# Kernel optimization log

Measured on AMD Instinct MI355X. Metric: run time of the kernel, lower is better.

The kernel has to match this reference:

```python
import jax, jax.numpy as jnp
import numpy as np
from jax import lax

IOU_THRESHOLD = 0.2  # hardcoded in TinyModel.forward
N = 8192


def setup_inputs() -> dict:
    key = jax.random.key(0)
    k1, k2, k3 = jax.random.split(key, 3)
    # Build valid boxes: top-left corner in [0, 1000), size in [1, 51)
    xy = jax.random.uniform(k1, (N, 2), dtype=jnp.float32) * 1000.0
    wh = jax.random.uniform(k2, (N, 2), dtype=jnp.float32) * 50.0 + 1.0
    rois = jnp.concatenate([xy, xy + wh], axis=-1)  # [N,4] = (x1,y1,x2,y2)
    scores = jax.random.uniform(k3, (N,), dtype=jnp.float32)
    return {"rois": rois, "scores": scores}


def _pairwise_iou(boxes):
    # boxes: [N,4]; returns [N,N] IoU (torchvision convention, no +1)
    x1, y1, x2, y2 = boxes[:, 0], boxes[:, 1], boxes[:, 2], boxes[:, 3]
    area = (x2 - x1) * (y2 - y1)                       # [N]
    ix1 = jnp.maximum(x1[:, None], x1[None, :])
    iy1 = jnp.maximum(y1[:, None], y1[None, :])
    ix2 = jnp.minimum(x2[:, None], x2[None, :])
    iy2 = jnp.minimum(y2[:, None], y2[None, :])
    iw = jnp.clip(ix2 - ix1, 0.0)
    ih = jnp.clip(iy2 - iy1, 0.0)
    inter = iw * ih                                    # [N,N]
    union = area[:, None] + area[None, :] - inter
    return inter / jnp.maximum(union, 1e-9)


def _nms_keep_mask(rois, scores, thr):
    n = rois.shape[0]
    order = jnp.argsort(-scores)                       # descending by score
    boxes = rois[order]                                # [N,4] sorted
    over = _pairwise_iou(boxes) > thr                  # [N,N] bool
    idx = jnp.arange(n)
    # box i may only suppress lower-scored boxes j > i (strict upper triangle)
    over = over & (idx[None, :] > idx[:, None])

    def body(i, keep):
        row = over[i] & keep[i]                        # suppress only if i survives
        return keep & ~row

    keep_sorted = lax.fori_loop(0, n, body, jnp.ones((n,), dtype=bool))
    # scatter back to original box ordering
    keep = jnp.zeros((n,), dtype=bool).at[order].set(keep_sorted)
    return keep


def reference(rois, scores):
    # NMS returns a data-dependent set of kept indices in torch; for fixed
    # shapes we return the scores with suppressed boxes zeroed (original order).
    keep = _nms_keep_mask(rois, scores, IOU_THRESHOLD)  # [N] bool
    return jnp.where(keep, scores, 0.0)
```

## Files before the change

kernel.cpp:

```cpp
#include <hip/hip_runtime.h>

#define N 8192
#define CAP 64
#define THR 0.2f

__global__ __launch_bounds__(256) void rank_kernel(const float* __restrict__ scores,
                                                   unsigned* __restrict__ rank) {
    __shared__ float s[1024];
    const int jbase = blockIdx.y * 1024;
    for (int t = threadIdx.x; t < 1024; t += 256) s[t] = scores[jbase + t];
    __syncthreads();
    const int i = blockIdx.x * 256 + threadIdx.x;
    const float si = scores[i];
    unsigned c = 0;
    #pragma unroll 8
    for (int jj = 0; jj < 1024; ++jj) {
        float sj = s[jj];
        int j = jbase + jj;
        c += (sj > si) || (sj == si && j < i);
    }
    atomicAdd(&rank[i], c);
}

__global__ __launch_bounds__(256) void scatter_kernel(const float* __restrict__ rois,
                                                      const unsigned* __restrict__ rank,
                                                      unsigned* __restrict__ order,
                                                      float4* __restrict__ sboxes) {
    const int i = blockIdx.x * 256 + threadIdx.x;
    const unsigned r = rank[i];
    order[r] = (unsigned)i;
    sboxes[r] = ((const float4*)rois)[i];
}

__device__ __forceinline__ bool iou_over(const float4 A, const float4 B) {
    float areaA = __fmul_rn(__fsub_rn(A.z, A.x), __fsub_rn(A.w, A.y));
    float areaB = __fmul_rn(__fsub_rn(B.z, B.x), __fsub_rn(B.w, B.y));
    float ix1 = fmaxf(A.x, B.x);
    float iy1 = fmaxf(A.y, B.y);
    float ix2 = fminf(A.z, B.z);
    float iy2 = fminf(A.w, B.w);
    float iw = fmaxf(__fsub_rn(ix2, ix1), 0.0f);
    float ih = fmaxf(__fsub_rn(iy2, iy1), 0.0f);
    float inter = __fmul_rn(iw, ih);
    float uni = __fsub_rn(__fadd_rn(areaA, areaB), inter);
    float iou = __fdiv_rn(inter, fmaxf(uni, 1e-9f));
    return iou > THR;
}

__global__ __launch_bounds__(256) void edge_kernel(const float4* __restrict__ sboxes,
                                                   unsigned long long* __restrict__ premask,
                                                   unsigned* __restrict__ cnt,
                                                   unsigned short* __restrict__ edgesTS,
                                                   unsigned short* __restrict__ edgesOvf) {
    const int k = blockIdx.x;
    int ti = (int)((257.0f - sqrtf(66049.0f - 8.0f * (float)k)) * 0.5f);
    if (ti > 127) ti = 127;
    if (ti < 0) ti = 0;
    while (ti < 127 && (128 * (ti + 1) - ((ti + 1) * ti) / 2) <= k) ++ti;
    while (ti > 0 && (128 * ti - (ti * (ti - 1)) / 2) > k) --ti;
    const int tj = ti + (k - (128 * ti - (ti * (ti - 1)) / 2));

    __shared__ float4 rb[64], cb[64];
    const int t = threadIdx.x;
    if (t < 64) rb[t] = sboxes[ti * 64 + t];
    else if (t < 128) cb[t - 64] = sboxes[tj * 64 + (t - 64)];
    __syncthreads();
    #pragma unroll
    for (int kk = 0; kk < 16; ++kk) {
        int p = kk * 256 + t;
        int r = p >> 6, c = p & 63;
        int is = ti * 64 + r, js = tj * 64 + c;
        if (js <= is) continue;
        if (iou_over(rb[r], cb[c])) {
            if (ti == tj) {
                atomicOr(&premask[js], 1ull << r);
            } else {
                unsigned pos = atomicAdd(&cnt[is], 1u);
                if (pos < 8) {
                    edgesTS[(((is >> 6) * 2 + (pos >> 2)) * 64 + (is & 63)) * 4 + (pos & 3)] =
                        (unsigned short)js;
                } else if (pos < CAP) {
                    edgesOvf[(size_t)is * 56 + (pos - 8)] = (unsigned short)js;
                }
            }
        }
    }
}


#define PF(B, CH) do { \
    int ch_ = (CH); \
    if (ch_ < 128) { \
        int pb_ = ch_ * 64 + lane; \
        pm##B = premask[pb_]; \
        n##B  = cnt[pb_]; \
        ea##B = edgesT[(ch_ * 2 + 0) * 64 + lane]; \
        eb##B = edgesT[(ch_ * 2 + 1) * 64 + lane]; \
    } \
} while (0)

#define APPLY(i, W, SH) { \
    unsigned d_ = (unsigned)((W) >> (SH)) & 0xFFFFu; \
    bool v_ = (i) < nn_; \
    unsigned a_ = v_ ? (d_ >> 5) : (unsigned)lane; \
    unsigned m_ = v_ ? ~(1u << (d_ & 31)) : ~0u; \
    atomicAnd(&alive[a_], m_); }

#define STEP(B, C) do { \
    const unsigned av_ = (alive[(C) * 2 + (lane >> 5)] >> (lane & 31)) & 1u; \
    unsigned long long anz = __ballot(pm##B != 0ull); \
    unsigned long long kept = __ballot(av_ != 0u); \
    if (anz != 0ull) { \
        bool mydec = !av_ || (pm##B == 0ull); \
        unsigned long long decided = __ballot(mydec); \
        kept = __ballot(av_ && (pm##B == 0ull)); \
        while (decided != ~0ull) { \
            bool ready = !mydec && ((pm##B & ~decided) == 0ull); \
            bool k_ = ready && ((pm##B & kept) == 0ull); \
            kept |= __ballot(k_); \
            decided |= __ballot(ready); \
            mydec = mydec || ready; \
        } \
    } \
    if (lane == 0) keptw[(C)] = kept; \
    const unsigned kb_ = (unsigned)(kept >> lane) & 1u; \
    unsigned nn_ = kb_ ? (n##B > 8u ? 8u : n##B) : 0u; \
    APPLY(0u, ea##B, 0)  APPLY(1u, ea##B, 16) APPLY(2u, ea##B, 32) APPLY(3u, ea##B, 48) \
    APPLY(4u, eb##B, 0)  APPLY(5u, eb##B, 16) APPLY(6u, eb##B, 32) APPLY(7u, eb##B, 48) \
    if (__any(kb_ && n##B > 8u)) { \
        unsigned nf_ = kb_ ? (n##B > CAP ? (unsigned)CAP : n##B) : 0u; \
        for (unsigned e_ = 8; e_ < nf_; ++e_) { \
            unsigned d_ = edgesOvf[(size_t)((C) * 64 + lane) * 56 + (e_ - 8)]; \
            atomicAnd(&alive[d_ >> 5], ~(1u << (d_ & 31))); \
        } \
    } \
    PF(B, (C) + 8); \
    asm volatile("s_waitcnt lgkmcnt(0)" ::: "memory"); \
} while (0)

__global__ __launch_bounds__(64) void resolve_kernel(const unsigned long long* __restrict__ premask,
                                                     const unsigned* __restrict__ cnt,
                                                     const unsigned long long* __restrict__ edgesT,
                                                     const unsigned short* __restrict__ edgesOvf,
                                                     unsigned long long* __restrict__ keptw) {
    __shared__ unsigned alive[256];
    const int lane = threadIdx.x;
    #pragma unroll
    for (int w = 0; w < 4; ++w) alive[w * 64 + lane] = 0xFFFFFFFFu;
    asm volatile("s_waitcnt lgkmcnt(0)" ::: "memory");

    unsigned long long pm0, pm1, pm2, pm3, pm4, pm5, pm6, pm7;
    unsigned n0, n1, n2, n3, n4, n5, n6, n7;
    unsigned long long ea0, ea1, ea2, ea3, ea4, ea5, ea6, ea7;
    unsigned long long eb0, eb1, eb2, eb3, eb4, eb5, eb6, eb7;

    PF(0, 0); PF(1, 1); PF(2, 2); PF(3, 3);
    PF(4, 4); PF(5, 5); PF(6, 6); PF(7, 7);

    for (int cc = 0; cc < 128; cc += 8) {
        STEP(0, cc + 0); STEP(1, cc + 1); STEP(2, cc + 2); STEP(3, cc + 3);
        STEP(4, cc + 4); STEP(5, cc + 5); STEP(6, cc + 6); STEP(7, cc + 7);
    }
}

__global__ __launch_bounds__(256) void out_kernel(const float* __restrict__ scores,
                                                  const unsigned* __restrict__ order,
                                                  const unsigned long long* __restrict__ keptw,
                                                  float* __restrict__ out) {
    const int s = blockIdx.x * 256 + threadIdx.x;
    const unsigned orig = order[s];
    const unsigned keep = (unsigned)((keptw[s >> 6] >> (s & 63)) & 1ull);
    out[orig] = keep ? scores[orig] : 0.0f;
}

extern "C" void kernel_launch(void* const* d_in, const int* in_sizes, int n_in,
                              void* d_out, int out_size, void* d_ws, size_t ws_size,
                              hipStream_t stream) {
    const float* rois   = (const float*)d_in[0];
    const float* scores = (const float*)d_in[1];
    float* out = (float*)d_out;

    char* ws = (char*)d_ws;
    unsigned*            rank     = (unsigned*)(ws);
    unsigned*            cnt      = (unsigned*)(ws + 32768);
    unsigned long long*  premask  = (unsigned long long*)(ws + 65536);
    unsigned*            order    = (unsigned*)(ws + 131072);
    float4*              sboxes   = (float4*)(ws + 163840);
    unsigned long long*  keptw    = (unsigned long long*)(ws + 294912);
    unsigned long long*  edgesT   = (unsigned long long*)(ws + 295936);
    unsigned short*      edgesOvf = (unsigned short*)(ws + 427008);

    hipMemsetAsync(ws, 0, 131072, stream);

    rank_kernel<<<dim3(32, 8), 256, 0, stream>>>(scores, rank);
    scatter_kernel<<<32, 256, 0, stream>>>(rois, rank, order, sboxes);
    edge_kernel<<<8256, 256, 0, stream>>>(sboxes, premask, cnt,
                                          (unsigned short*)edgesT, edgesOvf);
    resolve_kernel<<<1, 64, 0, stream>>>(premask, cnt, edgesT, edgesOvf, keptw);
    out_kernel<<<32, 256, 0, stream>>>(scores, order, keptw, out);
}
```

Baseline: 132.8 us.

## Fuse NMS pipeline into one persistent kernel with grid-wide barriers

Replaces the memset plus five separate launches (rank, scatter, edge, resolve, output) with a single persistent kernel of 512 blocks. Stages are separated by atomic-counter grid barriers, and workspace zeroing moves into the kernel. The rank and scatter steps are merged, and the final output write is folded into the single-wave resolve stage using a kept-mask held in shared memory. The aim is to remove launch and inter-kernel gaps. The cost is spin-waiting barriers, which assume all 512 blocks are co-resident. The output scatter is also now done by one wavefront instead of 32 blocks.

```diff
diff --git a/kernel.cpp b/kernel.cpp
--- a/kernel.cpp
+++ b/kernel.cpp
@@ -1,36 +1,10 @@
 #include <hip/hip_runtime.h>
 
 #define N 8192
+#define NBLK 512
 #define CAP 64
 #define THR 0.2f
 
-__global__ __launch_bounds__(256) void rank_kernel(const float* __restrict__ scores,
-                                                   unsigned* __restrict__ rank) {
-    __shared__ float s[1024];
-    const int jbase = blockIdx.y * 1024;
-    for (int t = threadIdx.x; t < 1024; t += 256) s[t] = scores[jbase + t];
-    __syncthreads();
-    const int i = blockIdx.x * 256 + threadIdx.x;
-    const float si = scores[i];
-    unsigned c = 0;
-    #pragma unroll 8
-    for (int jj = 0; jj < 1024; ++jj) {
-        float sj = s[jj];
-        int j = jbase + jj;
-        c += (sj > si) || (sj == si && j < i);
-    }
-    atomicAdd(&rank[i], c);
-}
-
-__global__ __launch_bounds__(256) void scatter_kernel(const float* __restrict__ rois,
-                                                      const unsigned* __restrict__ rank,
-                                                      unsigned* __restrict__ order,
-                                                      float4* __restrict__ sboxes) {
-    const int i = blockIdx.x * 256 + threadIdx.x;
-    const unsigned r = rank[i];
-    order[r] = (unsigned)i;
-    sboxes[r] = ((const float4*)rois)[i];
-}
 
 __device__ __forceinline__ bool iou_over(const float4 A, const float4 B) {
     float areaA = __fmul_rn(__fsub_rn(A.z, A.x), __fsub_rn(A.w, A.y));
@@ -47,52 +21,26 @@
     return iou > THR;
 }
 
-__global__ __launch_bounds__(256) void edge_kernel(const float4* __restrict__ sboxes,
-                                                   unsigned long long* __restrict__ premask,
-                                                   unsigned* __restrict__ cnt,
-                                                   unsigned short* __restrict__ edgesTS,
-                                                   unsigned short* __restrict__ edgesOvf) {
-    const int k = blockIdx.x;
-    int ti = (int)((257.0f - sqrtf(66049.0f - 8.0f * (float)k)) * 0.5f);
-    if (ti > 127) ti = 127;
-    if (ti < 0) ti = 0;
-    while (ti < 127 && (128 * (ti + 1) - ((ti + 1) * ti) / 2) <= k) ++ti;
-    while (ti > 0 && (128 * ti - (ti * (ti - 1)) / 2) > k) --ti;
-    const int tj = ti + (k - (128 * ti - (ti * (ti - 1)) / 2));
-
-    __shared__ float4 rb[64], cb[64];
-    const int t = threadIdx.x;
-    if (t < 64) rb[t] = sboxes[ti * 64 + t];
-    else if (t < 128) cb[t - 64] = sboxes[tj * 64 + (t - 64)];
+__device__ __forceinline__ void bar_arrive(unsigned* bar) {
+    __threadfence();
     __syncthreads();
-    #pragma unroll
-    for (int kk = 0; kk < 16; ++kk) {
-        int p = kk * 256 + t;
-        int r = p >> 6, c = p & 63;
-        int is = ti * 64 + r, js = tj * 64 + c;
-        if (js <= is) continue;
-        if (iou_over(rb[r], cb[c])) {
-            if (ti == tj) {
-                atomicOr(&premask[js], 1ull << r);
-            } else {
-                unsigned pos = atomicAdd(&cnt[is], 1u);
-                if (pos < 8) {
-                    edgesTS[(((is >> 6) * 2 + (pos >> 2)) * 64 + (is & 63)) * 4 + (pos & 3)] =
-                        (unsigned short)js;
-                } else if (pos < CAP) {
-                    edgesOvf[(size_t)is * 56 + (pos - 8)] = (unsigned short)js;
-                }
-            }
-        }
-    }
-}
-
+    if (threadIdx.x == 0)
+        __hip_atomic_fetch_add(bar, 1u, __ATOMIC_RELEASE, __HIP_MEMORY_SCOPE_AGENT);
+}
+__device__ __forceinline__ void bar_wait(unsigned* bar, unsigned target) {
+    if (threadIdx.x == 0) {
+        while (__hip_atomic_load(bar, __ATOMIC_ACQUIRE, __HIP_MEMORY_SCOPE_AGENT) < target)
+            __builtin_amdgcn_s_sleep(8);
+    }
+    __syncthreads();
+    (void)__hip_atomic_load(bar, __ATOMIC_ACQUIRE, __HIP_MEMORY_SCOPE_AGENT);
+}
 
 #define PF(B, CH) do { \
     int ch_ = (CH); \
     if (ch_ < 128) { \
         int pb_ = ch_ * 64 + lane; \
-        pm##B = premask[pb_]; \
+        pm##B = prem[pb_]; \
         n##B  = cnt[pb_]; \
         ea##B = edgesT[(ch_ * 2 + 0) * 64 + lane]; \
         eb##B = edgesT[(ch_ * 2 + 1) * 64 + lane]; \
@@ -122,7 +70,7 @@
             mydec = mydec || ready; \
         } \
     } \
-    if (lane == 0) keptw[(C)] = kept; \
+    if (lane == 0) keptL[(C)] = kept; \
     const unsigned kb_ = (unsigned)(kept >> lane) & 1u; \
     unsigned nn_ = kb_ ? (n##B > 8u ? 8u : n##B) : 0u; \
     APPLY(0u, ea##B, 0)  APPLY(1u, ea##B, 16) APPLY(2u, ea##B, 32) APPLY(3u, ea##B, 48) \
@@ -138,13 +86,110 @@
     asm volatile("s_waitcnt lgkmcnt(0)" ::: "memory"); \
 } while (0)
 
-__global__ __launch_bounds__(64) void resolve_kernel(const unsigned long long* __restrict__ premask,
-                                                     const unsigned* __restrict__ cnt,
-                                                     const unsigned long long* __restrict__ edgesT,
-                                                     const unsigned short* __restrict__ edgesOvf,
-                                                     unsigned long long* __restrict__ keptw) {
+__global__ __launch_bounds__(256, 2)
+void mega_kernel(const float* __restrict__ rois,
+                 const float* __restrict__ scores,
+                 float* __restrict__ out,
+                 unsigned* bar,
+                 unsigned* cnt,
+                 unsigned long long* prem,
+                 unsigned* order,
+                 float4* sboxes,
+                 unsigned long long* edgesT,
+                 unsigned short* edgesOvf) {
+    __shared__ float sc[1024];
+    __shared__ unsigned part[256];
+    __shared__ float4 rb[64], cb[64];
     __shared__ unsigned alive[256];
-    const int lane = threadIdx.x;
+    __shared__ unsigned long long keptL[128];
+
+    const int t = threadIdx.x;
+    const int b = blockIdx.x;
+    const int gtid = b * 256 + t;
+
+    {
+        unsigned* z = cnt;
+        if (gtid < 8192) z[gtid] = 0u;
+        unsigned* pz = (unsigned*)prem;
+        if (gtid < 16384) pz[gtid] = 0u;
+    }
+
+    {
+        const int ib  = b * 16;
+        const int il  = t >> 4;
+        const int i   = ib + il;
+        const int sub = t & 15;
+        const float si = scores[i];
+        unsigned c = 0;
+        for (int tile = 0; tile < 8; ++tile) {
+            ((float4*)sc)[t] = ((const float4*)scores)[tile * 256 + t];
+            __syncthreads();
+            const int j0 = sub * 64;
+            #pragma unroll 16
+            for (int q = 0; q < 64; ++q) {
+                int jj = j0 + q;
+                float sj = sc[jj];
+                int j = tile * 1024 + jj;
+                c += (sj > si) || (sj == si && j < i);
+            }
+            __syncthreads();
+        }
+        part[t] = c;
+        __syncthreads();
+        if (t < 16) {
+            const int i2 = ib + t;
+            unsigned r = 0;
+            #pragma unroll
+            for (int q = 0; q < 16; ++q) r += part[t * 16 + q];
+            order[r] = (unsigned)i2;
+            sboxes[r] = ((const float4*)rois)[i2];
+        }
+    }
+
+    bar_arrive(bar);
+    bar_wait(bar, NBLK);
+
+    unsigned short* edgesTS = (unsigned short*)edgesT;
+    for (int p = b; p < 8256; p += NBLK) {
+        int ti = (int)((257.0f - sqrtf(66049.0f - 8.0f * (float)p)) * 0.5f);
+        if (ti > 127) ti = 127;
+        if (ti < 0) ti = 0;
+        while (ti < 127 && (128 * (ti + 1) - ((ti + 1) * ti) / 2) <= p) ++ti;
+        while (ti > 0 && (128 * ti - (ti * (ti - 1)) / 2) > p) --ti;
+        const int tj = ti + (p - (128 * ti - (ti * (ti - 1)) / 2));
+
+        if (t < 64) rb[t] = sboxes[ti * 64 + t];
+        else if (t < 128) cb[t - 64] = sboxes[tj * 64 + (t - 64)];
+        __syncthreads();
+        #pragma unroll
+        for (int kk = 0; kk < 16; ++kk) {
+            int pp = kk * 256 + t;
+            int r = pp >> 6, c = pp & 63;
+            int is = ti * 64 + r, js = tj * 64 + c;
+            if (js <= is) continue;
+            if (iou_over(rb[r], cb[c])) {
+                if (ti == tj) {
+                    atomicOr(&prem[js], 1ull << r);
+                } else {
+                    unsigned pos = atomicAdd(&cnt[is], 1u);
+                    if (pos < 8) {
+                        edgesTS[(((is >> 6) * 2 + (pos >> 2)) * 64 + (is & 63)) * 4 + (pos & 3)] =
+                            (unsigned short)js;
+                    } else if (pos < CAP) {
+                        edgesOvf[(size_t)is * 56 + (pos - 8)] = (unsigned short)js;
+                    }
+                }
+            }
+        }
+        __syncthreads();
+    }
+
+    bar_arrive(bar);
+    if (b != 0) return;
+    bar_wait(bar, 2 * NBLK);
+    if (t >= 64) return;
+
+    const int lane = t;
     #pragma unroll
     for (int w = 0; w < 4; ++w) alive[w * 64 + lane] = 0xFFFFFFFFu;
     asm volatile("s_waitcnt lgkmcnt(0)" ::: "memory");
@@ -161,16 +206,15 @@
         STEP(0, cc + 0); STEP(1, cc + 1); STEP(2, cc + 2); STEP(3, cc + 3);
         STEP(4, cc + 4); STEP(5, cc + 5); STEP(6, cc + 6); STEP(7, cc + 7);
     }
-}
-
-__global__ __launch_bounds__(256) void out_kernel(const float* __restrict__ scores,
-                                                  const unsigned* __restrict__ order,
-                                                  const unsigned long long* __restrict__ keptw,
-                                                  float* __restrict__ out) {
-    const int s = blockIdx.x * 256 + threadIdx.x;
-    const unsigned orig = order[s];
-    const unsigned keep = (unsigned)((keptw[s >> 6] >> (s & 63)) & 1ull);
-    out[orig] = keep ? scores[orig] : 0.0f;
+
+    #pragma unroll 8
+    for (int q = 0; q < 128; ++q) {
+        int s = q * 64 + lane;
+        unsigned long long kw = keptL[q];
+        unsigned orig = order[s];
+        float v = ((kw >> lane) & 1ull) ? scores[orig] : 0.0f;
+        out[orig] = v;
+    }
 }
 
 extern "C" void kernel_launch(void* const* d_in, const int* in_sizes, int n_in,
@@ -181,21 +225,16 @@
     float* out = (float*)d_out;
 
     char* ws = (char*)d_ws;
-    unsigned*            rank     = (unsigned*)(ws);
-    unsigned*            cnt      = (unsigned*)(ws + 32768);
-    unsigned long long*  premask  = (unsigned long long*)(ws + 65536);
-    unsigned*            order    = (unsigned*)(ws + 131072);
-    float4*              sboxes   = (float4*)(ws + 163840);
-    unsigned long long*  keptw    = (unsigned long long*)(ws + 294912);
-    unsigned long long*  edgesT   = (unsigned long long*)(ws + 295936);
-    unsigned short*      edgesOvf = (unsigned short*)(ws + 427008);
-
-    hipMemsetAsync(ws, 0, 131072, stream);
-
-    rank_kernel<<<dim3(32, 8), 256, 0, stream>>>(scores, rank);
-    scatter_kernel<<<32, 256, 0, stream>>>(rois, rank, order, sboxes);
-    edge_kernel<<<8256, 256, 0, stream>>>(sboxes, premask, cnt,
-                                          (unsigned short*)edgesT, edgesOvf);
-    resolve_kernel<<<1, 64, 0, stream>>>(premask, cnt, edgesT, edgesOvf, keptw);
-    out_kernel<<<32, 256, 0, stream>>>(scores, order, keptw, out);
-}
+    unsigned*            bar      = (unsigned*)(ws);
+    unsigned*            cnt      = (unsigned*)(ws + 256);
+    unsigned long long*  prem     = (unsigned long long*)(ws + 33024);
+    unsigned*            order    = (unsigned*)(ws + 98560);
+    float4*              sboxes   = (float4*)(ws + 131328);
+    unsigned long long*  edgesT   = (unsigned long long*)(ws + 262400);
+    unsigned short*      edgesOvf = (unsigned short*)(ws + 393472);
+
+    hipMemsetAsync(ws, 0, 256, stream);
+
+    mega_kernel<<<NBLK, 256, 0, stream>>>(rois, scores, out, bar, cnt, prem,
+                                          order, sboxes, edgesT, edgesOvf);
+}
```

Result: slower. 312.3 us (+135.2%).

## Resolve 256-box groups via in-register bitmask chains and fuse output scatter

Applied to the files above, without the earlier changes.

Edges between boxes in the same 256-box group now go to a 4-word per-box bitmask instead of the sparse edge lists. The single-wave resolver can then handle four 64-box chunks per step, chaining kept masks with ballots rather than doing atomic alive-bit updates through LDS. It also removes one launch by folding the output kernel into the resolver. The costs are a larger memset, more work inside the serial single-wave kernel for the output pass, and higher register pressure.

```diff
diff --git a/kernel.cpp b/kernel.cpp
--- a/kernel.cpp
+++ b/kernel.cpp
@@ -3,6 +3,7 @@
 #define N 8192
 #define CAP 64
 #define THR 0.2f
+
 
 __global__ __launch_bounds__(256) void rank_kernel(const float* __restrict__ scores,
                                                    unsigned* __restrict__ rank) {
@@ -48,7 +49,7 @@
 }
 
 __global__ __launch_bounds__(256) void edge_kernel(const float4* __restrict__ sboxes,
-                                                   unsigned long long* __restrict__ premask,
+                                                   unsigned long long* __restrict__ prem,
                                                    unsigned* __restrict__ cnt,
                                                    unsigned short* __restrict__ edgesTS,
                                                    unsigned short* __restrict__ edgesOvf) {
@@ -65,15 +66,16 @@
     if (t < 64) rb[t] = sboxes[ti * 64 + t];
     else if (t < 128) cb[t - 64] = sboxes[tj * 64 + (t - 64)];
     __syncthreads();
+    const bool same256 = (ti >> 2) == (tj >> 2);
     #pragma unroll
     for (int kk = 0; kk < 16; ++kk) {
-        int p = kk * 256 + t;
-        int r = p >> 6, c = p & 63;
+        int pp = kk * 256 + t;
+        int r = pp >> 6, c = pp & 63;
         int is = ti * 64 + r, js = tj * 64 + c;
         if (js <= is) continue;
         if (iou_over(rb[r], cb[c])) {
-            if (ti == tj) {
-                atomicOr(&premask[js], 1ull << r);
+            if (same256) {
+                atomicOr(&prem[(size_t)js * 4 + ((is >> 6) & 3)], 1ull << (is & 63));
             } else {
                 unsigned pos = atomicAdd(&cnt[is], 1u);
                 if (pos < 8) {
@@ -87,15 +89,41 @@
     }
 }
 
-
-#define PF(B, CH) do { \
+__device__ __forceinline__ unsigned long long resolve_group(bool av, unsigned long long pmw) {
+    unsigned long long anz = __ballot(av && pmw != 0ull);
+    unsigned long long kept = __ballot(av);
+    if (anz != 0ull) {
+        bool mydec = !av || (pmw == 0ull);
+        unsigned long long decided = __ballot(mydec);
+        kept = __ballot(av && (pmw == 0ull));
+        while (decided != ~0ull) {
+            bool ready = !mydec && ((pmw & ~decided) == 0ull);
+            bool kk = ready && ((pmw & kept) == 0ull);
+            kept |= __ballot(kk);
+            decided |= __ballot(ready);
+            mydec = mydec || ready;
+        }
+    }
+    return kept;
+}
+
+#define PF(X, CH) do { \
     int ch_ = (CH); \
-    if (ch_ < 128) { \
-        int pb_ = ch_ * 64 + lane; \
-        pm##B = premask[pb_]; \
-        n##B  = cnt[pb_]; \
-        ea##B = edgesT[(ch_ * 2 + 0) * 64 + lane]; \
-        eb##B = edgesT[(ch_ * 2 + 1) * 64 + lane]; \
+    if (ch_ < 32) { \
+        int b0_ = ch_ * 256 + lane; \
+        const ulonglong2* p2_ = (const ulonglong2*)prem; \
+        pm0##X  = prem[(size_t)b0_ * 4]; \
+        pm1##X  = p2_[(size_t)(b0_ + 64) * 2]; \
+        pm2a##X = p2_[(size_t)(b0_ + 128) * 2]; \
+        pm2b##X = prem[(size_t)(b0_ + 128) * 4 + 2]; \
+        pm3a##X = p2_[(size_t)(b0_ + 192) * 2]; \
+        pm3b##X = p2_[(size_t)(b0_ + 192) * 2 + 1]; \
+        n0##X = cnt[b0_]; n1##X = cnt[b0_ + 64]; n2##X = cnt[b0_ + 128]; n3##X = cnt[b0_ + 192]; \
+        int g4_ = ch_ * 4; \
+        ea0##X = edgesT[((g4_ + 0) * 2 + 0) * 64 + lane]; eb0##X = edgesT[((g4_ + 0) * 2 + 1) * 64 + lane]; \
+        ea1##X = edgesT[((g4_ + 1) * 2 + 0) * 64 + lane]; eb1##X = edgesT[((g4_ + 1) * 2 + 1) * 64 + lane]; \
+        ea2##X = edgesT[((g4_ + 2) * 2 + 0) * 64 + lane]; eb2##X = edgesT[((g4_ + 2) * 2 + 1) * 64 + lane]; \
+        ea3##X = edgesT[((g4_ + 3) * 2 + 0) * 64 + lane]; eb3##X = edgesT[((g4_ + 3) * 2 + 1) * 64 + lane]; \
     } \
 } while (0)
 
@@ -106,71 +134,93 @@
     unsigned m_ = v_ ? ~(1u << (d_ & 31)) : ~0u; \
     atomicAnd(&alive[a_], m_); }
 
-#define STEP(B, C) do { \
-    const unsigned av_ = (alive[(C) * 2 + (lane >> 5)] >> (lane & 31)) & 1u; \
-    unsigned long long anz = __ballot(pm##B != 0ull); \
-    unsigned long long kept = __ballot(av_ != 0u); \
-    if (anz != 0ull) { \
-        bool mydec = !av_ || (pm##B == 0ull); \
-        unsigned long long decided = __ballot(mydec); \
-        kept = __ballot(av_ && (pm##B == 0ull)); \
-        while (decided != ~0ull) { \
-            bool ready = !mydec && ((pm##B & ~decided) == 0ull); \
-            bool k_ = ready && ((pm##B & kept) == 0ull); \
-            kept |= __ballot(k_); \
-            decided |= __ballot(ready); \
-            mydec = mydec || ready; \
-        } \
+#define OVFG(KB, NV, BB) { \
+    unsigned nf_ = (KB) ? ((NV) > (unsigned)CAP ? (unsigned)CAP : (NV)) : 0u; \
+    for (unsigned e_ = 8; e_ < nf_; ++e_) { \
+        unsigned d_ = edgesOvf[(size_t)(BB) * 56 + (e_ - 8)]; \
+        atomicAnd(&alive[d_ >> 5], ~(1u << (d_ & 31))); } }
+
+#define STEP(X, C) do { \
+    unsigned aw0_ = alive[(C) * 8 + 0 + (lane >> 5)]; \
+    unsigned aw1_ = alive[(C) * 8 + 2 + (lane >> 5)]; \
+    unsigned aw2_ = alive[(C) * 8 + 4 + (lane >> 5)]; \
+    unsigned aw3_ = alive[(C) * 8 + 6 + (lane >> 5)]; \
+    const unsigned sh_ = lane & 31; \
+    bool av0_ = (aw0_ >> sh_) & 1u; \
+    unsigned long long k0_ = resolve_group(av0_, pm0##X); \
+    bool av1_ = ((aw1_ >> sh_) & 1u) && ((pm1##X.x & k0_) == 0ull); \
+    unsigned long long k1_ = resolve_group(av1_, pm1##X.y); \
+    bool av2_ = ((aw2_ >> sh_) & 1u) && (((pm2a##X.x & k0_) | (pm2a##X.y & k1_)) == 0ull); \
+    unsigned long long k2_ = resolve_group(av2_, pm2b##X); \
+    bool av3_ = ((aw3_ >> sh_) & 1u) && (((pm3a##X.x & k0_) | (pm3a##X.y & k1_) | (pm3b##X.x & k2_)) == 0ull); \
+    unsigned long long k3_ = resolve_group(av3_, pm3b##X.y); \
+    if (lane == 0) { \
+        keptL[(C) * 4 + 0] = k0_; keptL[(C) * 4 + 1] = k1_; \
+        keptL[(C) * 4 + 2] = k2_; keptL[(C) * 4 + 3] = k3_; \
     } \
-    if (lane == 0) keptw[(C)] = kept; \
-    const unsigned kb_ = (unsigned)(kept >> lane) & 1u; \
-    unsigned nn_ = kb_ ? (n##B > 8u ? 8u : n##B) : 0u; \
-    APPLY(0u, ea##B, 0)  APPLY(1u, ea##B, 16) APPLY(2u, ea##B, 32) APPLY(3u, ea##B, 48) \
-    APPLY(4u, eb##B, 0)  APPLY(5u, eb##B, 16) APPLY(6u, eb##B, 32) APPLY(7u, eb##B, 48) \
-    if (__any(kb_ && n##B > 8u)) { \
-        unsigned nf_ = kb_ ? (n##B > CAP ? (unsigned)CAP : n##B) : 0u; \
-        for (unsigned e_ = 8; e_ < nf_; ++e_) { \
-            unsigned d_ = edgesOvf[(size_t)((C) * 64 + lane) * 56 + (e_ - 8)]; \
-            atomicAnd(&alive[d_ >> 5], ~(1u << (d_ & 31))); \
-        } \
+    unsigned kb0_ = (unsigned)(k0_ >> lane) & 1u; \
+    unsigned kb1_ = (unsigned)(k1_ >> lane) & 1u; \
+    unsigned kb2_ = (unsigned)(k2_ >> lane) & 1u; \
+    unsigned kb3_ = (unsigned)(k3_ >> lane) & 1u; \
+    unsigned nn_; \
+    nn_ = kb0_ ? (n0##X > 8u ? 8u : n0##X) : 0u; \
+    APPLY(0u, ea0##X, 0)  APPLY(1u, ea0##X, 16) APPLY(2u, ea0##X, 32) APPLY(3u, ea0##X, 48) \
+    APPLY(4u, eb0##X, 0)  APPLY(5u, eb0##X, 16) APPLY(6u, eb0##X, 32) APPLY(7u, eb0##X, 48) \
+    nn_ = kb1_ ? (n1##X > 8u ? 8u : n1##X) : 0u; \
+    APPLY(0u, ea1##X, 0)  APPLY(1u, ea1##X, 16) APPLY(2u, ea1##X, 32) APPLY(3u, ea1##X, 48) \
+    APPLY(4u, eb1##X, 0)  APPLY(5u, eb1##X, 16) APPLY(6u, eb1##X, 32) APPLY(7u, eb1##X, 48) \
+    nn_ = kb2_ ? (n2##X > 8u ? 8u : n2##X) : 0u; \
+    APPLY(0u, ea2##X, 0)  APPLY(1u, ea2##X, 16) APPLY(2u, ea2##X, 32) APPLY(3u, ea2##X, 48) \
+    APPLY(4u, eb2##X, 0)  APPLY(5u, eb2##X, 16) APPLY(6u, eb2##X, 32) APPLY(7u, eb2##X, 48) \
+    nn_ = kb3_ ? (n3##X > 8u ? 8u : n3##X) : 0u; \
+    APPLY(0u, ea3##X, 0)  APPLY(1u, ea3##X, 16) APPLY(2u, ea3##X, 32) APPLY(3u, ea3##X, 48) \
+    APPLY(4u, eb3##X, 0)  APPLY(5u, eb3##X, 16) APPLY(6u, eb3##X, 32) APPLY(7u, eb3##X, 48) \
+    if (__any((kb0_ && n0##X > 8u) || (kb1_ && n1##X > 8u) || \
+              (kb2_ && n2##X > 8u) || (kb3_ && n3##X > 8u))) { \
+        OVFG(kb0_, n0##X, (C) * 256 + lane) \
+        OVFG(kb1_, n1##X, (C) * 256 + 64 + lane) \
+        OVFG(kb2_, n2##X, (C) * 256 + 128 + lane) \
+        OVFG(kb3_, n3##X, (C) * 256 + 192 + lane) \
     } \
-    PF(B, (C) + 8); \
+    PF(X, (C) + 2); \
     asm volatile("s_waitcnt lgkmcnt(0)" ::: "memory"); \
 } while (0)
 
-__global__ __launch_bounds__(64) void resolve_kernel(const unsigned long long* __restrict__ premask,
-                                                     const unsigned* __restrict__ cnt,
-                                                     const unsigned long long* __restrict__ edgesT,
-                                                     const unsigned short* __restrict__ edgesOvf,
-                                                     unsigned long long* __restrict__ keptw) {
+__global__ __launch_bounds__(64)
+void resolve_out_kernel(const unsigned long long* __restrict__ prem,
+                        const unsigned* __restrict__ cnt,
+                        const unsigned long long* __restrict__ edgesT,
+                        const unsigned short* __restrict__ edgesOvf,
+                        const unsigned* __restrict__ order,
+                        const float* __restrict__ scores,
+                        float* __restrict__ out) {
     __shared__ unsigned alive[256];
+    __shared__ unsigned long long keptL[128];
     const int lane = threadIdx.x;
     #pragma unroll
     for (int w = 0; w < 4; ++w) alive[w * 64 + lane] = 0xFFFFFFFFu;
     asm volatile("s_waitcnt lgkmcnt(0)" ::: "memory");
 
-    unsigned long long pm0, pm1, pm2, pm3, pm4, pm5, pm6, pm7;
-    unsigned n0, n1, n2, n3, n4, n5, n6, n7;
-    unsigned long long ea0, ea1, ea2, ea3, ea4, ea5, ea6, ea7;
-    unsigned long long eb0, eb1, eb2, eb3, eb4, eb5, eb6, eb7;
-
-    PF(0, 0); PF(1, 1); PF(2, 2); PF(3, 3);
-    PF(4, 4); PF(5, 5); PF(6, 6); PF(7, 7);
-
-    for (int cc = 0; cc < 128; cc += 8) {
-        STEP(0, cc + 0); STEP(1, cc + 1); STEP(2, cc + 2); STEP(3, cc + 3);
-        STEP(4, cc + 4); STEP(5, cc + 5); STEP(6, cc + 6); STEP(7, cc + 7);
-    }
-}
-
-__global__ __launch_bounds__(256) void out_kernel(const float* __restrict__ scores,
-                                                  const unsigned* __restrict__ order,
-                                                  const unsigned long long* __restrict__ keptw,
-                                                  float* __restrict__ out) {
-    const int s = blockIdx.x * 256 + threadIdx.x;
-    const unsigned orig = order[s];
-    const unsigned keep = (unsigned)((keptw[s >> 6] >> (s & 63)) & 1ull);
-    out[orig] = keep ? scores[orig] : 0.0f;
+    unsigned long long pm0A, pm2bA, pm0B, pm2bB;
+    ulonglong2 pm1A, pm2aA, pm3aA, pm3bA, pm1B, pm2aB, pm3aB, pm3bB;
+    unsigned n0A, n1A, n2A, n3A, n0B, n1B, n2B, n3B;
+    unsigned long long ea0A, eb0A, ea1A, eb1A, ea2A, eb2A, ea3A, eb3A;
+    unsigned long long ea0B, eb0B, ea1B, eb1B, ea2B, eb2B, ea3B, eb3B;
+
+    PF(A, 0); PF(B, 1);
+
+    for (int cc = 0; cc < 32; cc += 2) {
+        STEP(A, cc);
+        STEP(B, cc + 1);
+    }
+
+    #pragma unroll 4
+    for (int q = 0; q < 128; ++q) {
+        int s = q * 64 + lane;
+        unsigned long long kw = keptL[q];
+        unsigned orig = order[s];
+        out[orig] = ((kw >> lane) & 1ull) ? scores[orig] : 0.0f;
+    }
 }
 
 extern "C" void kernel_launch(void* const* d_in, const int* in_sizes, int n_in,
@@ -183,19 +233,18 @@
     char* ws = (char*)d_ws;
     unsigned*            rank     = (unsigned*)(ws);
     unsigned*            cnt      = (unsigned*)(ws + 32768);
-    unsigned long long*  premask  = (unsigned long long*)(ws + 65536);
-    unsigned*            order    = (unsigned*)(ws + 131072);
-    float4*              sboxes   = (float4*)(ws + 163840);
-    unsigned long long*  keptw    = (unsigned long long*)(ws + 294912);
-    unsigned long long*  edgesT   = (unsigned long long*)(ws + 295936);
-    unsigned short*      edgesOvf = (unsigned short*)(ws + 427008);
-
-    hipMemsetAsync(ws, 0, 131072, stream);
+    unsigned long long*  prem     = (unsigned long long*)(ws + 65536);
+    unsigned*            order    = (unsigned*)(ws + 327680);
+    float4*              sboxes   = (float4*)(ws + 360448);
+    unsigned long long*  edgesT   = (unsigned long long*)(ws + 491520);
+    unsigned short*      edgesOvf = (unsigned short*)(ws + 622592);
+
+    hipMemsetAsync(ws, 0, 327680, stream);
 
     rank_kernel<<<dim3(32, 8), 256, 0, stream>>>(scores, rank);
     scatter_kernel<<<32, 256, 0, stream>>>(rois, rank, order, sboxes);
-    edge_kernel<<<8256, 256, 0, stream>>>(sboxes, premask, cnt,
+    edge_kernel<<<8256, 256, 0, stream>>>(sboxes, prem, cnt,
                                           (unsigned short*)edgesT, edgesOvf);
-    resolve_kernel<<<1, 64, 0, stream>>>(premask, cnt, edgesT, edgesOvf, keptw);
-    out_kernel<<<32, 256, 0, stream>>>(scores, order, keptw, out);
-}
+    resolve_out_kernel<<<1, 64, 0, stream>>>(prem, cnt, edgesT, edgesOvf,
+                                             order, scores, out);
+}
```

Result: slower. 160.0 us (+20.5%).

## Fuse rank and scatter kernels, zero workspace in-kernel, drop memset

Applied to the files above, without the earlier changes.

Merges rank computation and scatter into one kernel. Each box is ranked by 8 threads that reduce their counts with shuffles instead of global atomics, and the sorted order and boxes are written directly. The workspace zeroing is moved from a separate memset into the same kernel, which removes two launches (memset and scatter) from the serial chain. The trade-off is that each block now loops over all 8192 scores, and the workspace is relaid out.

```diff
diff --git a/kernel.cpp b/kernel.cpp
--- a/kernel.cpp
+++ b/kernel.cpp
@@ -4,32 +4,41 @@
 #define CAP 64
 #define THR 0.2f
 
-__global__ __launch_bounds__(256) void rank_kernel(const float* __restrict__ scores,
-                                                   unsigned* __restrict__ rank) {
-    __shared__ float s[1024];
-    const int jbase = blockIdx.y * 1024;
-    for (int t = threadIdx.x; t < 1024; t += 256) s[t] = scores[jbase + t];
-    __syncthreads();
-    const int i = blockIdx.x * 256 + threadIdx.x;
+
+__global__ __launch_bounds__(256) void rank_scatter_kernel(const float* __restrict__ rois,
+                                                           const float* __restrict__ scores,
+                                                           uint4* __restrict__ zbase,
+                                                           unsigned* __restrict__ order,
+                                                           float4* __restrict__ sboxes) {
+    __shared__ float sc[1024];
+    const int t = threadIdx.x, b = blockIdx.x;
+
+    const int g = b * 256 + t;
+    if (g < 6144) zbase[g] = make_uint4(0, 0, 0, 0);
+
+    const int il = t >> 3, sub = t & 7;
+    const int i = b * 32 + il;
     const float si = scores[i];
     unsigned c = 0;
-    #pragma unroll 8
-    for (int jj = 0; jj < 1024; ++jj) {
-        float sj = s[jj];
-        int j = jbase + jj;
-        c += (sj > si) || (sj == si && j < i);
-    }
-    atomicAdd(&rank[i], c);
-}
-
-__global__ __launch_bounds__(256) void scatter_kernel(const float* __restrict__ rois,
-                                                      const unsigned* __restrict__ rank,
-                                                      unsigned* __restrict__ order,
-                                                      float4* __restrict__ sboxes) {
-    const int i = blockIdx.x * 256 + threadIdx.x;
-    const unsigned r = rank[i];
-    order[r] = (unsigned)i;
-    sboxes[r] = ((const float4*)rois)[i];
+    for (int tile = 0; tile < 8; ++tile) {
+        ((float4*)sc)[t] = ((const float4*)scores)[tile * 256 + t];
+        __syncthreads();
+        #pragma unroll 16
+        for (int q = 0; q < 128; ++q) {
+            int jj = q * 8 + sub;
+            float sj = sc[jj];
+            int j = tile * 1024 + jj;
+            c += (sj > si) || (sj == si && j < i);
+        }
+        __syncthreads();
+    }
+    c += __shfl_xor(c, 1);
+    c += __shfl_xor(c, 2);
+    c += __shfl_xor(c, 4);
+    if (sub == 0) {
+        order[c] = (unsigned)i;
+        sboxes[c] = ((const float4*)rois)[i];
+    }
 }
 
 __device__ __forceinline__ bool iou_over(const float4 A, const float4 B) {
@@ -67,8 +76,8 @@
     __syncthreads();
     #pragma unroll
     for (int kk = 0; kk < 16; ++kk) {
-        int p = kk * 256 + t;
-        int r = p >> 6, c = p & 63;
+        int pp = kk * 256 + t;
+        int r = pp >> 6, c = pp & 63;
         int is = ti * 64 + r, js = tj * 64 + c;
         if (js <= is) continue;
         if (iou_over(rb[r], cb[c])) {
@@ -86,7 +95,6 @@
         }
     }
 }
-
 
 #define PF(B, CH) do { \
     int ch_ = (CH); \
@@ -138,11 +146,12 @@
     asm volatile("s_waitcnt lgkmcnt(0)" ::: "memory"); \
 } while (0)
 
-__global__ __launch_bounds__(64) void resolve_kernel(const unsigned long long* __restrict__ premask,
-                                                     const unsigned* __restrict__ cnt,
-                                                     const unsigned long long* __restrict__ edgesT,
-                                                     const unsigned short* __restrict__ edgesOvf,
-                                                     unsigned long long* __restrict__ keptw) {
+__global__ __launch_bounds__(64, 1)
+void resolve_kernel(const unsigned long long* __restrict__ premask,
+                    const unsigned* __restrict__ cnt,
+                    const unsigned long long* __restrict__ edgesT,
+                    const unsigned short* __restrict__ edgesOvf,
+                    unsigned long long* __restrict__ keptw) {
     __shared__ unsigned alive[256];
     const int lane = threadIdx.x;
     #pragma unroll
@@ -181,19 +190,15 @@
     float* out = (float*)d_out;
 
     char* ws = (char*)d_ws;
-    unsigned*            rank     = (unsigned*)(ws);
-    unsigned*            cnt      = (unsigned*)(ws + 32768);
-    unsigned long long*  premask  = (unsigned long long*)(ws + 65536);
-    unsigned*            order    = (unsigned*)(ws + 131072);
-    float4*              sboxes   = (float4*)(ws + 163840);
-    unsigned long long*  keptw    = (unsigned long long*)(ws + 294912);
-    unsigned long long*  edgesT   = (unsigned long long*)(ws + 295936);
-    unsigned short*      edgesOvf = (unsigned short*)(ws + 427008);
-
-    hipMemsetAsync(ws, 0, 131072, stream);
-
-    rank_kernel<<<dim3(32, 8), 256, 0, stream>>>(scores, rank);
-    scatter_kernel<<<32, 256, 0, stream>>>(rois, rank, order, sboxes);
+    unsigned*            cnt      = (unsigned*)(ws);
+    unsigned long long*  premask  = (unsigned long long*)(ws + 32768);
+    unsigned*            order    = (unsigned*)(ws + 98304);
+    float4*              sboxes   = (float4*)(ws + 131072);
+    unsigned long long*  edgesT   = (unsigned long long*)(ws + 262144);
+    unsigned short*      edgesOvf = (unsigned short*)(ws + 393216);
+    unsigned long long*  keptw    = (unsigned long long*)(ws + 1310720);
+
+    rank_scatter_kernel<<<256, 256, 0, stream>>>(rois, scores, (uint4*)ws, order, sboxes);
     edge_kernel<<<8256, 256, 0, stream>>>(sboxes, premask, cnt,
                                           (unsigned short*)edgesT, edgesOvf);
     resolve_kernel<<<1, 64, 0, stream>>>(premask, cnt, edgesT, edgesOvf, keptw);
```

After: 134.6 us. Within noise of the previous version (+1.4%).
